# Kernel optimization log

Hardware: AMD Instinct MI355X
Metric: run time of the kernel (lower is better)

## Reference

```python
import jax, jax.numpy as jnp
import numpy as np

N = 63001
F_IN = 512
F_OUT = 256
E = 2_000_000
LRELU_ALPHA = 0.2


def setup_inputs() -> dict:
    key = jax.random.key(0)
    ks = jax.random.split(key, 10)
    x = jax.random.normal(ks[0], (N, F_IN), dtype=jnp.float32)
    values = jax.random.uniform(ks[1], (E,), dtype=jnp.float32)
    edge_index = jax.random.randint(ks[2], (2, E), 0, N, dtype=jnp.int32)
    # learned params: conv1d kernel_size=1 == dense matmuls
    W = jax.random.normal(ks[3], (F_IN, F_OUT), dtype=jnp.float32) * (1.0 / np.sqrt(F_IN))
    a1 = jax.random.normal(ks[4], (F_OUT,), dtype=jnp.float32) * (1.0 / np.sqrt(F_OUT))
    b1 = jnp.zeros((), dtype=jnp.float32)
    a2 = jax.random.normal(ks[5], (F_OUT,), dtype=jnp.float32) * (1.0 / np.sqrt(F_OUT))
    b2 = jnp.zeros((), dtype=jnp.float32)
    b_out = jnp.zeros((F_OUT,), dtype=jnp.float32)
    return {"x": x, "values": values, "edge_index": edge_index,
            "W": W, "a1": a1, "b1": b1, "a2": a2, "b2": b2, "b_out": b_out}


def reference(x, values, edge_index, W, a1, b1, a2, b2, b_out):
    src = edge_index[0]  # row index i of sparse adjacency entry
    dst = edge_index[1]  # col index j

    # conv1d(kernel=1) projections == matmuls
    seq_fts = x @ W                      # [N, F_out]
    f1 = seq_fts @ a1 + b1               # [N]
    f2 = seq_fts @ a2 + b2               # [N]

    # edgewise logits: s_ij * f1_i + s_ij * f2_j  (sparse_add of two masked broadcasts)
    logits = values * (f1[src] + f2[dst])           # [E]
    logits = jax.nn.leaky_relu(logits, LRELU_ALPHA)

    # sparse row-wise softmax over edges grouped by src
    m = jax.ops.segment_max(logits, src, num_segments=N)   # [N]
    p = jnp.exp(logits - m[src])                            # [E]
    denom = jax.ops.segment_sum(p, src, num_segments=N)     # [N]
    coefs = p / denom[src]                                  # [E]

    # SPMM: out_i = sum_j coef_ij * seq_fts_j
    out = jnp.zeros((N, F_OUT), dtype=seq_fts.dtype)
    out = out.at[src].add(coefs[:, None] * seq_fts[dst])

    out = out + b_out                                       # bias_add
    return jax.nn.elu(out)
```

## Files before the change

### kernel.cpp

```cpp
#include <hip/hip_runtime.h>
#include <hip/hip_bf16.h>
#include <cstdint>
#include <cstddef>

#define FIN 512
#define FOUT 256
#define LRELU 0.2f
#define NBKT 16
#define BSH 12

typedef __attribute__((ext_vector_type(8))) short bf16x8;
typedef __attribute__((ext_vector_type(8))) unsigned short u16x8;
typedef __attribute__((ext_vector_type(4))) float f32x4;
typedef _Float16 h16x2 __attribute__((ext_vector_type(2)));

#define PERM_LO 0x05040100u
#define PERM_HI 0x07060302u
#define ONE2H   0x3C003C00u

__device__ inline ushort f2bf(float f) {
    __hip_bfloat16 h = __float2bfloat16(f);
    union { __hip_bfloat16 h; ushort u; } c; c.h = h;
    return c.u;
}
__device__ inline ushort f2h(float f) {
    union { _Float16 h; ushort u; } c; c.h = (_Float16)f;
    return c.u;
}
__device__ inline h16x2 u2h2(uint32_t u) {
    union { uint32_t u; h16x2 h; } c; c.u = u;
    return c.h;
}
__device__ inline float hdot2(h16x2 pp, uint32_t sv, float acc) {
    return __builtin_amdgcn_fdot2(pp, u2h2(sv), acc, false);
}

__global__ void prep_wt(const float* __restrict__ W, ushort* __restrict__ WT)
{
    const int idx = blockIdx.x * blockDim.x + threadIdx.x;
    if (idx < FIN * FOUT) {
        const int k = idx >> 8, n = idx & 255;
        WT[(size_t)n * FIN + k] = f2bf(W[(size_t)k * FOUT + n]);
    }
}

#define BM 128
#define BK 64
__global__ __launch_bounds__(512) void gemm_bf16(
    const float* __restrict__ A, const ushort* __restrict__ BT,
    ushort* __restrict__ Ch,
    const float* __restrict__ a1, const float* __restrict__ a2,
    const float* __restrict__ b1, const float* __restrict__ b2,
    float* __restrict__ f1, float* __restrict__ f2,
    int M)
{
    __shared__ ushort As[BM * BK];
    __shared__ ushort Bs[FOUT * BK];
    __shared__ float f1s[BM][2];
    __shared__ float f2s[BM][2];
    const int t = threadIdx.x;
    const int lane = t & 63, w = t >> 6;
    const int wm = w & 3, wn = w >> 2;
    const int brow = blockIdx.x * BM;

    f32x4 acc[2][8] = {};

    const int ar = t >> 2;
    const int ak = (t & 3) << 4;

    const int bcol8 = (lane >> 3);
    const int bslot = lane & 7;
    const int bcdat = bslot ^ (bcol8 & 7);

    for (int k0 = 0; k0 < FIN; k0 += BK) {
#pragma unroll
        for (int j = 0; j < 4; ++j) {
            const int grp = w * 4 + j;
            const int col = grp * 8 + bcol8;
            const ushort* gsrc = BT + (size_t)col * FIN + k0 + bcdat * 8;
            ushort* ldst = &Bs[grp * 512];
            __builtin_amdgcn_global_load_lds(
                (const __attribute__((address_space(1))) void*)gsrc,
                (__attribute__((address_space(3))) void*)ldst, 16, 0, 0);
        }
        {
            f32x4 v0, v1, v2, v3;
            const int grow = brow + ar;
            if (grow < M) {
                const f32x4* p = (const f32x4*)(A + (size_t)grow * FIN + k0 + ak);
                v0 = __builtin_nontemporal_load(p + 0);
                v1 = __builtin_nontemporal_load(p + 1);
                v2 = __builtin_nontemporal_load(p + 2);
                v3 = __builtin_nontemporal_load(p + 3);
            } else {
                v0 = v1 = v2 = v3 = (f32x4)0.f;
            }
            u16x8 w0, w1;
            w0[0]=f2bf(v0[0]); w0[1]=f2bf(v0[1]); w0[2]=f2bf(v0[2]); w0[3]=f2bf(v0[3]);
            w0[4]=f2bf(v1[0]); w0[5]=f2bf(v1[1]); w0[6]=f2bf(v1[2]); w0[7]=f2bf(v1[3]);
            w1[0]=f2bf(v2[0]); w1[1]=f2bf(v2[1]); w1[2]=f2bf(v2[2]); w1[3]=f2bf(v2[3]);
            w1[4]=f2bf(v3[0]); w1[5]=f2bf(v3[1]); w1[6]=f2bf(v3[2]); w1[7]=f2bf(v3[3]);
            const int c0 = ((ak >> 3) + 0) ^ (ar & 7);
            const int c1 = ((ak >> 3) + 1) ^ (ar & 7);
            *(u16x8*)(&As[ar * BK + (c0 << 3)]) = w0;
            *(u16x8*)(&As[ar * BK + (c1 << 3)]) = w1;
        }
        __syncthreads();

#pragma unroll
        for (int kk = 0; kk < 2; ++kk) {
            const int kc = kk * 4 + (lane >> 4);
            bf16x8 af[2], bfr[8];
#pragma unroll
            for (int m = 0; m < 2; ++m) {
                const int row = wm * 32 + m * 16 + (lane & 15);
                af[m] = *(const bf16x8*)(&As[row * BK + ((kc ^ (row & 7)) << 3)]);
            }
#pragma unroll
            for (int n = 0; n < 8; ++n) {
                const int col = wn * 128 + n * 16 + (lane & 15);
                bfr[n] = *(const bf16x8*)(&Bs[col * BK + ((kc ^ (col & 7)) << 3)]);
            }
#pragma unroll
            for (int m = 0; m < 2; ++m)
#pragma unroll
                for (int n = 0; n < 8; ++n)
                    acc[m][n] = __builtin_amdgcn_mfma_f32_16x16x32_bf16(
                        af[m], bfr[n], acc[m][n], 0, 0, 0);
        }
        __syncthreads();
    }

    float a1c[8], a2c[8];
#pragma unroll
    for (int n = 0; n < 8; ++n) {
        const int col = wn * 128 + n * 16 + (lane & 15);
        a1c[n] = a1[col];
        a2c[n] = a2[col];
    }
    const int cbase = wn * 128 + (lane & 15);
#pragma unroll
    for (int m = 0; m < 2; ++m) {
#pragma unroll
        for (int reg = 0; reg < 4; ++reg) {
            const int rloc = wm * 32 + m * 16 + (lane >> 4) * 4 + reg;
            const int r = brow + rloc;
            float p1 = 0.f, p2 = 0.f;
#pragma unroll
            for (int n = 0; n < 8; ++n) {
                p1 += acc[m][n][reg] * a1c[n];
                p2 += acc[m][n][reg] * a2c[n];
            }
#pragma unroll
            for (int off = 1; off < 16; off <<= 1) {
                p1 += __shfl_xor(p1, off);
                p2 += __shfl_xor(p2, off);
            }
            if ((lane & 15) == 0) {
                f1s[rloc][wn] = p1;
                f2s[rloc][wn] = p2;
            }
            if (r < M) {
#pragma unroll
                for (int n = 0; n < 8; ++n)
                    Ch[(size_t)r * FOUT + cbase + n * 16] = f2h(acc[m][n][reg]);
            }
        }
    }
    __syncthreads();
    if (t < BM) {
        const int r = brow + t;
        if (r < M) {
            f1[r] = f1s[t][0] + f1s[t][1] + b1[0];
            f2[r] = f2s[t][0] + f2s[t][1] + b2[0];
        }
    }
}

__global__ void pos_kernel(const int* __restrict__ src, const int* __restrict__ dst,
                           int* __restrict__ cnt, ushort* __restrict__ pos, int E)
{
    int i = (blockIdx.x * blockDim.x + threadIdx.x) * 4;
    if (i + 4 <= E) {
        const int4 s = *(const int4*)(src + i);
        const int4 d = *(const int4*)(dst + i);
        ushort4 p;
        p.x = (ushort)atomicAdd(&cnt[s.x * NBKT + (d.x >> BSH)], 1);
        p.y = (ushort)atomicAdd(&cnt[s.y * NBKT + (d.y >> BSH)], 1);
        p.z = (ushort)atomicAdd(&cnt[s.z * NBKT + (d.z >> BSH)], 1);
        p.w = (ushort)atomicAdd(&cnt[s.w * NBKT + (d.w >> BSH)], 1);
        *(ushort4*)(pos + i) = p;
    } else {
        for (; i < E; ++i)
            pos[i] = (ushort)atomicAdd(&cnt[src[i] * NBKT + (dst[i] >> BSH)], 1);
    }
}

__global__ __launch_bounds__(1024) void scan_blk(const int* __restrict__ cnt,
                                                 int* __restrict__ btot, int K)
{
    __shared__ int s[1024];
    const int t = threadIdx.x;
    const int idx = blockIdx.x * 1024 + t;
    s[t] = (idx < K) ? cnt[idx] : 0;
    __syncthreads();
    for (int off = 512; off; off >>= 1) {
        if (t < off) s[t] += s[t + off];
        __syncthreads();
    }
    if (t == 0) btot[blockIdx.x] = s[0];
}

__global__ __launch_bounds__(1024) void scan_top(const int* __restrict__ btot,
                                                 int* __restrict__ boff, int nb)
{
    __shared__ int s[1024];
    const int t = threadIdx.x;
    const int mine = (t < nb) ? btot[t] : 0;
    s[t] = mine;
    __syncthreads();
    for (int off = 1; off < 1024; off <<= 1) {
        const int u = (t >= off) ? s[t - off] : 0;
        __syncthreads();
        s[t] += u;
        __syncthreads();
    }
    if (t < nb) boff[t] = s[t] - mine;
}

__global__ __launch_bounds__(1024) void scan_out(const int* __restrict__ cnt,
                                                 const int* __restrict__ boff,
                                                 int* __restrict__ koff, int K)
{
    __shared__ int s[1024];
    const int t = threadIdx.x;
    const int b = blockIdx.x;
    const int idx = b * 1024 + t;
    const int v = (idx < K) ? cnt[idx] : 0;
    s[t] = v;
    __syncthreads();
    for (int off = 1; off < 1024; off <<= 1) {
        const int u = (t >= off) ? s[t - off] : 0;
        __syncthreads();
        s[t] += u;
        __syncthreads();
    }
    if (idx < K)      koff[idx] = boff[b] + s[t] - v;
    if (idx == K - 1) koff[K]   = boff[b] + s[t];
}

__global__ void scatter_p(const int* __restrict__ src, const int* __restrict__ dst,
                          const float* __restrict__ values, const ushort* __restrict__ pos,
                          const float* __restrict__ f1, const float* __restrict__ f2,
                          const int* __restrict__ koff,
                          uint32_t* __restrict__ pd, int E)
{
    const int i = blockIdx.x * blockDim.x + threadIdx.x;
    if (i < E) {
        const int s = src[i];
        const int d = dst[i];
        float lg = values[i] * (f1[s] + f2[d]);
        lg = (lg > 0.f) ? lg : LRELU * lg;
        const float p = __expf(lg);
        const int slot = koff[s * NBKT + (d >> BSH)] + (int)pos[i];
        __builtin_nontemporal_store(((uint32_t)d << 16) | (uint32_t)f2h(p), &pd[slot]);
    }
}

__global__ __launch_bounds__(256) void spmm_kernel(
    const ushort* __restrict__ seq,
    const uint32_t* __restrict__ pd,
    const int* __restrict__ koff, const float* __restrict__ b_out,
    float* __restrict__ out, int N)
{
    const int w = threadIdx.x >> 6, lane = threadIdx.x & 63;
    const int row = blockIdx.x * 4 + w;
    if (row >= N) return;
    const int start = __builtin_amdgcn_readfirstlane(koff[row * NBKT]);
    const int end   = __builtin_amdgcn_readfirstlane(koff[(row + 1) * NBKT]);

    const ushort* seql = seq + lane * 4;
    float acc0 = 0.f, acc1 = 0.f, acc2 = 0.f, acc3 = 0.f, den = 0.f;

    int t = start;
    for (; t + 8 <= end; t += 8) {
        uint32_t q[8];
#pragma unroll
        for (int j = 0; j < 8; ++j) q[j] = pd[t + j];
        uint2 s[8];
#pragma unroll
        for (int j = 0; j < 8; ++j)
            s[j] = *(const uint2*)(seql + (size_t)(q[j] >> 16) * FOUT);
#pragma unroll
        for (int j = 0; j < 8; j += 2) {
            const h16x2 pp = u2h2((q[j] & 0xffffu) | (q[j + 1] << 16));
            acc0 = hdot2(pp, __builtin_amdgcn_perm(s[j+1].x, s[j].x, PERM_LO), acc0);
            acc1 = hdot2(pp, __builtin_amdgcn_perm(s[j+1].x, s[j].x, PERM_HI), acc1);
            acc2 = hdot2(pp, __builtin_amdgcn_perm(s[j+1].y, s[j].y, PERM_LO), acc2);
            acc3 = hdot2(pp, __builtin_amdgcn_perm(s[j+1].y, s[j].y, PERM_HI), acc3);
            den  = hdot2(pp, ONE2H, den);
        }
    }
    for (; t + 2 <= end; t += 2) {
        const uint32_t q0 = pd[t], q1 = pd[t + 1];
        const uint2 s0 = *(const uint2*)(seql + (size_t)(q0 >> 16) * FOUT);
        const uint2 s1 = *(const uint2*)(seql + (size_t)(q1 >> 16) * FOUT);
        const h16x2 pp = u2h2((q0 & 0xffffu) | (q1 << 16));
        acc0 = hdot2(pp, __builtin_amdgcn_perm(s1.x, s0.x, PERM_LO), acc0);
        acc1 = hdot2(pp, __builtin_amdgcn_perm(s1.x, s0.x, PERM_HI), acc1);
        acc2 = hdot2(pp, __builtin_amdgcn_perm(s1.y, s0.y, PERM_LO), acc2);
        acc3 = hdot2(pp, __builtin_amdgcn_perm(s1.y, s0.y, PERM_HI), acc3);
        den  = hdot2(pp, ONE2H, den);
    }
    if (t < end) {
        const uint32_t q0 = pd[t];
        const uint2 s0 = *(const uint2*)(seql + (size_t)(q0 >> 16) * FOUT);
        const h16x2 pp = u2h2(q0 & 0xffffu);
        acc0 = hdot2(pp, __builtin_amdgcn_perm(s0.x, s0.x, PERM_LO), acc0);
        acc1 = hdot2(pp, __builtin_amdgcn_perm(s0.x, s0.x, PERM_HI), acc1);
        acc2 = hdot2(pp, __builtin_amdgcn_perm(s0.y, s0.y, PERM_LO), acc2);
        acc3 = hdot2(pp, __builtin_amdgcn_perm(s0.y, s0.y, PERM_HI), acc3);
        den  = hdot2(pp, ONE2H, den);
    }

    const float inv = (end > start) ? 1.f / den : 0.f;
    const float4 bo = *(const float4*)(b_out + lane * 4);
    f32x4 o;
    o[0] = acc0 * inv + bo.x;
    o[1] = acc1 * inv + bo.y;
    o[2] = acc2 * inv + bo.z;
    o[3] = acc3 * inv + bo.w;
    o[0] = (o[0] > 0.f) ? o[0] : expm1f(o[0]);
    o[1] = (o[1] > 0.f) ? o[1] : expm1f(o[1]);
    o[2] = (o[2] > 0.f) ? o[2] : expm1f(o[2]);
    o[3] = (o[3] > 0.f) ? o[3] : expm1f(o[3]);
    __builtin_nontemporal_store(o, (f32x4*)(out + (size_t)row * FOUT + lane * 4));
}

extern "C" void kernel_launch(void* const* d_in, const int* in_sizes, int n_in,
                              void* d_out, int out_size, void* d_ws, size_t ws_size,
                              hipStream_t stream)
{
    const float* x      = (const float*)d_in[0];
    const float* values = (const float*)d_in[1];
    const int*   ei     = (const int*)d_in[2];
    const float* W      = (const float*)d_in[3];
    const float* a1     = (const float*)d_in[4];
    const float* b1     = (const float*)d_in[5];
    const float* a2     = (const float*)d_in[6];
    const float* b2     = (const float*)d_in[7];
    const float* b_out  = (const float*)d_in[8];
    float* out = (float*)d_out;

    const int N = in_sizes[0] / FIN;
    const int E = in_sizes[1];
    const int* src = ei;
    const int* dst = ei + E;
    const int K = N * NBKT;

    auto alignup = [](size_t v) { return (v + 255) & ~(size_t)255; };
    char* ws = (char*)d_ws;
    size_t off = 0;
    ushort*   seqh = (ushort*)(ws + off);   off = alignup(off + (size_t)N * FOUT * 2);
    ushort*   WT   = (ushort*)(ws + off);   off = alignup(off + (size_t)FIN * FOUT * 2);
    float*    f1   = (float*)(ws + off);    off = alignup(off + (size_t)N * 4);
    float*    f2   = (float*)(ws + off);    off = alignup(off + (size_t)N * 4);
    int*      cnt  = (int*)(ws + off);      off = alignup(off + (size_t)K * 4);
    int*      koff = (int*)(ws + off);      off = alignup(off + (size_t)(K + 1) * 4);
    int*      btot = (int*)(ws + off);      off = alignup(off + (size_t)1024 * 4);
    int*      boff = (int*)(ws + off);      off = alignup(off + (size_t)1024 * 4);
    ushort*   pos  = (ushort*)(ws + off);   off = alignup(off + (size_t)E * 2);
    uint32_t* pd   = (uint32_t*)(ws + off); off = alignup(off + (size_t)E * 4);
    (void)ws_size;

    const int nbk = (K + 1023) / 1024;

    hipMemsetAsync(cnt, 0, (size_t)K * 4, stream);

    pos_kernel<<<(E / 4 + 255) / 256, 256, 0, stream>>>(src, dst, cnt, pos, E);
    scan_blk<<<nbk, 1024, 0, stream>>>(cnt, btot, K);
    scan_top<<<1, 1024, 0, stream>>>(btot, boff, nbk);
    scan_out<<<nbk, 1024, 0, stream>>>(cnt, boff, koff, K);

    prep_wt<<<(FIN * FOUT + 255) / 256, 256, 0, stream>>>(W, WT);
    gemm_bf16<<<(N + BM - 1) / BM, 512, 0, stream>>>(x, WT, seqh, a1, a2, b1, b2,
                                                     f1, f2, N);

    scatter_p<<<(E + 255) / 256, 256, 0, stream>>>(src, dst, values, pos, f1, f2,
                                                   koff, pd, E);

    spmm_kernel<<<(N + 3) / 4, 256, 0, stream>>>(seqh, pd, koff, b_out, out, N);
}
```

Measured before the change: 350.8 us.

## Drop dst bucketing in CSR build, fuse W prep, prefetch GEMM A tiles

New measurement: 331.4 us. 5.5% less time.

```diff
diff --git a/kernel.cpp b/kernel.cpp
--- a/kernel.cpp
+++ b/kernel.cpp
@@ -6,8 +6,6 @@
 #define FIN 512
 #define FOUT 256
 #define LRELU 0.2f
-#define NBKT 16
-#define BSH 12
 
 typedef __attribute__((ext_vector_type(8))) short bf16x8;
 typedef __attribute__((ext_vector_type(8))) unsigned short u16x8;
@@ -35,12 +33,29 @@
     return __builtin_amdgcn_fdot2(pp, u2h2(sv), acc, false);
 }
 
-__global__ void prep_wt(const float* __restrict__ W, ushort* __restrict__ WT)
-{
-    const int idx = blockIdx.x * blockDim.x + threadIdx.x;
-    if (idx < FIN * FOUT) {
-        const int k = idx >> 8, n = idx & 255;
-        WT[(size_t)n * FIN + k] = f2bf(W[(size_t)k * FOUT + n]);
+__global__ void pos_kernel(const int* __restrict__ src, int* __restrict__ cnt,
+                           ushort* __restrict__ pos, int E, int posBlks,
+                           const float* __restrict__ W, ushort* __restrict__ WT)
+{
+    if ((int)blockIdx.x >= posBlks) {
+        const int idx = ((int)blockIdx.x - posBlks) * 256 + threadIdx.x;
+        if (idx < FIN * FOUT) {
+            const int k = idx >> 8, n = idx & 255;
+            WT[(size_t)n * FIN + k] = f2bf(W[(size_t)k * FOUT + n]);
+        }
+        return;
+    }
+    int i = (blockIdx.x * blockDim.x + threadIdx.x) * 4;
+    if (i + 4 <= E) {
+        const int4 s = *(const int4*)(src + i);
+        ushort4 p;
+        p.x = (ushort)atomicAdd(&cnt[s.x], 1);
+        p.y = (ushort)atomicAdd(&cnt[s.y], 1);
+        p.z = (ushort)atomicAdd(&cnt[s.z], 1);
+        p.w = (ushort)atomicAdd(&cnt[s.w], 1);
+        *(ushort4*)(pos + i) = p;
+    } else {
+        for (; i < E; ++i) pos[i] = (ushort)atomicAdd(&cnt[src[i]], 1);
     }
 }
 
@@ -67,10 +82,24 @@
 
     const int ar = t >> 2;
     const int ak = (t & 3) << 4;
+    const int grow = brow + ar;
+    const bool arow_ok = (grow < M);
+    const float* aptr = A + (size_t)grow * FIN + ak;
 
     const int bcol8 = (lane >> 3);
     const int bslot = lane & 7;
     const int bcdat = bslot ^ (bcol8 & 7);
+
+    f32x4 va0, va1, va2, va3;
+    if (arow_ok) {
+        const f32x4* p = (const f32x4*)aptr;
+        va0 = __builtin_nontemporal_load(p + 0);
+        va1 = __builtin_nontemporal_load(p + 1);
+        va2 = __builtin_nontemporal_load(p + 2);
+        va3 = __builtin_nontemporal_load(p + 3);
+    } else {
+        va0 = va1 = va2 = va3 = (f32x4)0.f;
+    }
 
     for (int k0 = 0; k0 < FIN; k0 += BK) {
 #pragma unroll
@@ -84,28 +113,27 @@
                 (__attribute__((address_space(3))) void*)ldst, 16, 0, 0);
         }
         {
-            f32x4 v0, v1, v2, v3;
-            const int grow = brow + ar;
-            if (grow < M) {
-                const f32x4* p = (const f32x4*)(A + (size_t)grow * FIN + k0 + ak);
-                v0 = __builtin_nontemporal_load(p + 0);
-                v1 = __builtin_nontemporal_load(p + 1);
-                v2 = __builtin_nontemporal_load(p + 2);
-                v3 = __builtin_nontemporal_load(p + 3);
-            } else {
-                v0 = v1 = v2 = v3 = (f32x4)0.f;
-            }
             u16x8 w0, w1;
-            w0[0]=f2bf(v0[0]); w0[1]=f2bf(v0[1]); w0[2]=f2bf(v0[2]); w0[3]=f2bf(v0[3]);
-            w0[4]=f2bf(v1[0]); w0[5]=f2bf(v1[1]); w0[6]=f2bf(v1[2]); w0[7]=f2bf(v1[3]);
-            w1[0]=f2bf(v2[0]); w1[1]=f2bf(v2[1]); w1[2]=f2bf(v2[2]); w1[3]=f2bf(v2[3]);
-            w1[4]=f2bf(v3[0]); w1[5]=f2bf(v3[1]); w1[6]=f2bf(v3[2]); w1[7]=f2bf(v3[3]);
+            w0[0]=f2bf(va0[0]); w0[1]=f2bf(va0[1]); w0[2]=f2bf(va0[2]); w0[3]=f2bf(va0[3]);
+            w0[4]=f2bf(va1[0]); w0[5]=f2bf(va1[1]); w0[6]=f2bf(va1[2]); w0[7]=f2bf(va1[3]);
+            w1[0]=f2bf(va2[0]); w1[1]=f2bf(va2[1]); w1[2]=f2bf(va2[2]); w1[3]=f2bf(va2[3]);
+            w1[4]=f2bf(va3[0]); w1[5]=f2bf(va3[1]); w1[6]=f2bf(va3[2]); w1[7]=f2bf(va3[3]);
             const int c0 = ((ak >> 3) + 0) ^ (ar & 7);
             const int c1 = ((ak >> 3) + 1) ^ (ar & 7);
             *(u16x8*)(&As[ar * BK + (c0 << 3)]) = w0;
             *(u16x8*)(&As[ar * BK + (c1 << 3)]) = w1;
         }
         __syncthreads();
+
+        if (k0 + BK < FIN) {
+            if (arow_ok) {
+                const f32x4* p = (const f32x4*)(aptr + k0 + BK);
+                va0 = __builtin_nontemporal_load(p + 0);
+                va1 = __builtin_nontemporal_load(p + 1);
+                va2 = __builtin_nontemporal_load(p + 2);
+                va3 = __builtin_nontemporal_load(p + 3);
+            }
+        }
 
 #pragma unroll
         for (int kk = 0; kk < 2; ++kk) {
@@ -174,25 +202,6 @@
             f1[r] = f1s[t][0] + f1s[t][1] + b1[0];
             f2[r] = f2s[t][0] + f2s[t][1] + b2[0];
         }
-    }
-}
-
-__global__ void pos_kernel(const int* __restrict__ src, const int* __restrict__ dst,
-                           int* __restrict__ cnt, ushort* __restrict__ pos, int E)
-{
-    int i = (blockIdx.x * blockDim.x + threadIdx.x) * 4;
-    if (i + 4 <= E) {
-        const int4 s = *(const int4*)(src + i);
-        const int4 d = *(const int4*)(dst + i);
-        ushort4 p;
-        p.x = (ushort)atomicAdd(&cnt[s.x * NBKT + (d.x >> BSH)], 1);
-        p.y = (ushort)atomicAdd(&cnt[s.y * NBKT + (d.y >> BSH)], 1);
-        p.z = (ushort)atomicAdd(&cnt[s.z * NBKT + (d.z >> BSH)], 1);
-        p.w = (ushort)atomicAdd(&cnt[s.w * NBKT + (d.w >> BSH)], 1);
-        *(ushort4*)(pos + i) = p;
-    } else {
-        for (; i < E; ++i)
-            pos[i] = (ushort)atomicAdd(&cnt[src[i] * NBKT + (dst[i] >> BSH)], 1);
     }
 }
 
@@ -211,21 +220,18 @@
     if (t == 0) btot[blockIdx.x] = s[0];
 }
 
-__global__ __launch_bounds__(1024) void scan_top(const int* __restrict__ btot,
-                                                 int* __restrict__ boff, int nb)
-{
-    __shared__ int s[1024];
+__global__ __launch_bounds__(64) void scan_top(const int* __restrict__ btot,
+                                               int* __restrict__ boff, int nb)
+{
     const int t = threadIdx.x;
     const int mine = (t < nb) ? btot[t] : 0;
-    s[t] = mine;
-    __syncthreads();
-    for (int off = 1; off < 1024; off <<= 1) {
-        const int u = (t >= off) ? s[t - off] : 0;
-        __syncthreads();
-        s[t] += u;
-        __syncthreads();
-    }
-    if (t < nb) boff[t] = s[t] - mine;
+    int v = mine;
+#pragma unroll
+    for (int off = 1; off < 64; off <<= 1) {
+        const int u = __shfl_up(v, off);
+        if (t >= off) v += u;
+    }
+    if (t < nb) boff[t] = v - mine;
 }
 
 __global__ __launch_bounds__(1024) void scan_out(const int* __restrict__ cnt,
@@ -262,8 +268,8 @@
         float lg = values[i] * (f1[s] + f2[d]);
         lg = (lg > 0.f) ? lg : LRELU * lg;
         const float p = __expf(lg);
-        const int slot = koff[s * NBKT + (d >> BSH)] + (int)pos[i];
-        __builtin_nontemporal_store(((uint32_t)d << 16) | (uint32_t)f2h(p), &pd[slot]);
+        const int slot = koff[s] + (int)pos[i];
+        pd[slot] = ((uint32_t)d << 16) | (uint32_t)f2h(p);
     }
 }
 
@@ -276,8 +282,8 @@
     const int w = threadIdx.x >> 6, lane = threadIdx.x & 63;
     const int row = blockIdx.x * 4 + w;
     if (row >= N) return;
-    const int start = __builtin_amdgcn_readfirstlane(koff[row * NBKT]);
-    const int end   = __builtin_amdgcn_readfirstlane(koff[(row + 1) * NBKT]);
+    const int start = __builtin_amdgcn_readfirstlane(koff[row]);
+    const int end   = __builtin_amdgcn_readfirstlane(koff[row + 1]);
 
     const ushort* seql = seq + lane * 4;
     float acc0 = 0.f, acc1 = 0.f, acc2 = 0.f, acc3 = 0.f, den = 0.f;
@@ -356,7 +362,6 @@
     const int E = in_sizes[1];
     const int* src = ei;
     const int* dst = ei + E;
-    const int K = N * NBKT;
 
     auto alignup = [](size_t v) { return (v + 255) & ~(size_t)255; };
     char* ws = (char*)d_ws;
@@ -365,24 +370,25 @@
     ushort*   WT   = (ushort*)(ws + off);   off = alignup(off + (size_t)FIN * FOUT * 2);
     float*    f1   = (float*)(ws + off);    off = alignup(off + (size_t)N * 4);
     float*    f2   = (float*)(ws + off);    off = alignup(off + (size_t)N * 4);
-    int*      cnt  = (int*)(ws + off);      off = alignup(off + (size_t)K * 4);
-    int*      koff = (int*)(ws + off);      off = alignup(off + (size_t)(K + 1) * 4);
-    int*      btot = (int*)(ws + off);      off = alignup(off + (size_t)1024 * 4);
-    int*      boff = (int*)(ws + off);      off = alignup(off + (size_t)1024 * 4);
+    int*      cnt  = (int*)(ws + off);      off = alignup(off + (size_t)N * 4);
+    int*      koff = (int*)(ws + off);      off = alignup(off + (size_t)(N + 1) * 4);
+    int*      btot = (int*)(ws + off);      off = alignup(off + (size_t)64 * 4);
+    int*      boff = (int*)(ws + off);      off = alignup(off + (size_t)64 * 4);
     ushort*   pos  = (ushort*)(ws + off);   off = alignup(off + (size_t)E * 2);
     uint32_t* pd   = (uint32_t*)(ws + off); off = alignup(off + (size_t)E * 4);
     (void)ws_size;
 
-    const int nbk = (K + 1023) / 1024;
-
-    hipMemsetAsync(cnt, 0, (size_t)K * 4, stream);
-
-    pos_kernel<<<(E / 4 + 255) / 256, 256, 0, stream>>>(src, dst, cnt, pos, E);
-    scan_blk<<<nbk, 1024, 0, stream>>>(cnt, btot, K);
-    scan_top<<<1, 1024, 0, stream>>>(btot, boff, nbk);
-    scan_out<<<nbk, 1024, 0, stream>>>(cnt, boff, koff, K);
-
-    prep_wt<<<(FIN * FOUT + 255) / 256, 256, 0, stream>>>(W, WT);
+    const int nb = (N + 1023) / 1024;
+    const int posBlks = (E / 4 + 255) / 256;
+    const int prepBlks = (FIN * FOUT + 255) / 256;
+
+    hipMemsetAsync(cnt, 0, (size_t)N * 4, stream);
+
+    pos_kernel<<<posBlks + prepBlks, 256, 0, stream>>>(src, cnt, pos, E, posBlks, W, WT);
+    scan_blk<<<nb, 1024, 0, stream>>>(cnt, btot, N);
+    scan_top<<<1, 64, 0, stream>>>(btot, boff, nb);
+    scan_out<<<nb, 1024, 0, stream>>>(cnt, boff, koff, N);
+
     gemm_bf16<<<(N + BM - 1) / BM, 512, 0, stream>>>(x, WT, seqh, a1, a2, b1, b2,
                                                      f1, f2, N);
 
```
